# Optimization experiments

Measured on AMD Instinct MI355X. Metric: run time of the kernel, lower is better.

The kernel has to match this reference:

```python
import jax, jax.numpy as jnp
import numpy as np

B, K, C = 512, 64, 2048  # batch, mixture components, copy (eval points)


def setup_inputs() -> dict:
    key = jax.random.key(0)
    kw, km, ks, kr, kx = jax.random.split(key, 5)
    w = jax.random.uniform(kw, (B, K), dtype=jnp.float32)            # mixture weights
    means = jax.random.normal(km, (B, K, 2), dtype=jnp.float32)      # mean1, mean2
    sds = jax.random.uniform(ks, (B, K, 2), dtype=jnp.float32,
                             minval=0.5, maxval=1.5)                 # sd1, sd2 (>0)
    corr = jax.random.uniform(kr, (B, K), dtype=jnp.float32,
                              minval=-0.8, maxval=0.8)               # |corr| < 1
    model_out = jnp.concatenate(
        [w[..., None], means, sds, corr[..., None]], axis=-1)        # [B, K, 6]
    X = jax.random.normal(kx, (B, C, 2), dtype=jnp.float32)
    return {"model_out": model_out, "X": X}


def reference(model_out, X):
    # Unpack params: w, mean1, mean2, sd1, sd2, corr  -- each [B, K]
    w = model_out[..., 0]
    m1 = model_out[..., 1]
    m2 = model_out[..., 2]
    s1 = model_out[..., 3]
    s2 = model_out[..., 4]
    r = model_out[..., 5]

    # Closed-form bivariate normal pdf (equivalent to Cholesky-based
    # MultivariateNormal log_prob for the 2x2 covariance built in torch).
    # dx, dy: [B, C, K] via broadcasting X[B,C,1] against params[B,1,K]
    dx = (X[:, :, 0:1] - m1[:, None, :]) / s1[:, None, :]
    dy = (X[:, :, 1:2] - m2[:, None, :]) / s2[:, None, :]
    rb = r[:, None, :]
    omr2 = 1.0 - rb * rb  # 1 - rho^2
    z = dx * dx - 2.0 * rb * dx * dy + dy * dy
    two_pi = 2.0 * jnp.pi
    norm = two_pi * s1[:, None, :] * s2[:, None, :] * jnp.sqrt(omr2)
    probs = jnp.exp(-0.5 * z / omr2) / norm  # [B, C, K]

    # Weighted sum over components -> [B, C]
    return jnp.einsum('bck,bk->bc', probs, w)
```

## Files before the change

kernel.cpp:

```cpp
#include <hip/hip_runtime.h>
#include <hip/hip_bf16.h>


typedef float v2f __attribute__((ext_vector_type(2)));

constexpr int B = 512;
constexpr int K = 64;
constexpr int C = 2048;
constexpr int BLOCK = 256;
constexpr int HALVES = 2;
constexpr int CH = C / HALVES;

__global__ __launch_bounds__(256) void prep_kernel(
    const float* __restrict__ mo,
    float* __restrict__ P)
{
    const int i = blockIdx.x * 256 + threadIdx.x;
    const float* p = mo + (size_t)i * 6;
    const float w  = p[0];
    const float m1 = p[1];
    const float m2 = p[2];
    const float s1 = p[3];
    const float s2 = p[4];
    const float r  = p[5];

    const float omr2 = fmaf(-r, r, 1.0f);
    const float inv  = 1.0f / omr2;
    const float a2   = 0.7213475204444817f * inv;
    const float sc   = sqrtf(a2);
    const float is1  = sc / s1;
    const float is2  = sc / s2;
    const float nm1  = -(m1 * is1);
    const float nm2  = -(m2 * is2);
    const float r2   = 2.0f * r;
    const float wn   = w * 0.15915494309189535f / (s1 * s2 * sqrtf(omr2));

    float4* q = (float4*)(P + (size_t)i * 16);
    q[0] = make_float4(is1, is1, is2, is2);
    q[1] = make_float4(nm1, nm1, nm2, nm2);
    q[2] = make_float4(r2, r2, wn, wn);
}

__global__ __launch_bounds__(BLOCK) void mixture_kernel(
    const float* __restrict__ X,
    const float* __restrict__ P,
    float* __restrict__ out)
{
    const int bid = blockIdx.x;
    const int b   = bid >> 1;
    const int h   = bid & 1;
    const int t   = threadIdx.x;

    const float4* Xb = (const float4*)(X + (size_t)b * C * 2 + (size_t)h * CH * 2);
    const float4 xv0 = Xb[t];
    const float4 xv1 = Xb[t + BLOCK];

    const v2f xs0 = { xv0.x, xv0.z };
    const v2f ys0 = { xv0.y, xv0.w };
    const v2f xs1 = { xv1.x, xv1.z };
    const v2f ys1 = { xv1.y, xv1.w };
    v2f acc0 = { 0.0f, 0.0f };
    v2f acc1 = { 0.0f, 0.0f };

    const v2f* __restrict__ Pb = (const v2f*)(P + (size_t)b * K * 16);

#pragma unroll 4
    for (int k = 0; k < K; ++k) {
        const v2f IS1 = Pb[k * 8 + 0];
        const v2f IS2 = Pb[k * 8 + 1];
        const v2f NM1 = Pb[k * 8 + 2];
        const v2f NM2 = Pb[k * 8 + 3];
        const v2f R2  = Pb[k * 8 + 4];
        const v2f WN  = Pb[k * 8 + 5];

        {
            const v2f dx = __builtin_elementwise_fma(xs0, IS1, NM1);
            const v2f dy = __builtin_elementwise_fma(ys0, IS2, NM2);
            const v2f pq = dx * dy;
            v2f u        = dx * dx;
            u            = __builtin_elementwise_fma(dy, dy, u);
            const v2f e  = __builtin_elementwise_fma(R2, pq, -u);
            v2f ex;
            ex.x = __builtin_amdgcn_exp2f(e.x);
            ex.y = __builtin_amdgcn_exp2f(e.y);
            acc0 = __builtin_elementwise_fma(WN, ex, acc0);
        }
        {
            const v2f dx = __builtin_elementwise_fma(xs1, IS1, NM1);
            const v2f dy = __builtin_elementwise_fma(ys1, IS2, NM2);
            const v2f pq = dx * dy;
            v2f u        = dx * dx;
            u            = __builtin_elementwise_fma(dy, dy, u);
            const v2f e  = __builtin_elementwise_fma(R2, pq, -u);
            v2f ex;
            ex.x = __builtin_amdgcn_exp2f(e.x);
            ex.y = __builtin_amdgcn_exp2f(e.y);
            acc1 = __builtin_elementwise_fma(WN, ex, acc1);
        }
    }

    float2* ob = (float2*)(out + (size_t)b * C + (size_t)h * CH);
    ob[t]         = make_float2(acc0.x, acc0.y);
    ob[t + BLOCK] = make_float2(acc1.x, acc1.y);
}

extern "C" void kernel_launch(void* const* d_in, const int* in_sizes, int n_in,
                              void* d_out, int out_size, void* d_ws, size_t ws_size,
                              hipStream_t stream) {
    const float* mo = (const float*)d_in[0];
    const float* X  = (const float*)d_in[1];
    float* out      = (float*)d_out;
    float* P        = (float*)d_ws;

    prep_kernel<<<dim3(B * K / 256), dim3(256), 0, stream>>>(mo, P);
    mixture_kernel<<<dim3(B * HALVES), dim3(BLOCK), 0, stream>>>(X, P, out);
}
```

Baseline: 79.64 us.

## Fuse parameter prep into mixture kernel and broadcast params via readlane

Removes the separate prep kernel and its workspace round-trip: each wavefront lane computes the derived parameters for one mixture component, and the inner loop broadcasts them with readlane into scalar registers. This eliminates one kernel launch and the global-memory loads of the packed parameter table. In exchange every wave redundantly recomputes the 64 components' parameters (divisions, sqrts), and the loop unroll is raised to 8.

```diff
diff --git a/kernel.cpp b/kernel.cpp
--- a/kernel.cpp
+++ b/kernel.cpp
@@ -1,5 +1,4 @@
 #include <hip/hip_runtime.h>
-#include <hip/hip_bf16.h>
 
 
 typedef float v2f __attribute__((ext_vector_type(2)));
@@ -11,12 +10,26 @@
 constexpr int HALVES = 2;
 constexpr int CH = C / HALVES;
 
-__global__ __launch_bounds__(256) void prep_kernel(
+__device__ __forceinline__ float rdlane(float v, int k) {
+    return __uint_as_float(__builtin_amdgcn_readlane(__float_as_uint(v), k));
+}
+
+__global__ __launch_bounds__(BLOCK) void mixture_kernel(
     const float* __restrict__ mo,
-    float* __restrict__ P)
+    const float* __restrict__ X,
+    float* __restrict__ out)
 {
-    const int i = blockIdx.x * 256 + threadIdx.x;
-    const float* p = mo + (size_t)i * 6;
+    const int bid = blockIdx.x;
+    const int b   = bid >> 1;
+    const int h   = bid & 1;
+    const int t   = threadIdx.x;
+    const int lane = t & 63;
+
+    const float4* Xb = (const float4*)(X + (size_t)b * C * 2 + (size_t)h * CH * 2);
+    const float4 xv0 = Xb[t];
+    const float4 xv1 = Xb[t + BLOCK];
+
+    const float* p = mo + ((size_t)(b * K + lane)) * 6;
     const float w  = p[0];
     const float m1 = p[1];
     const float m2 = p[2];
@@ -28,32 +41,12 @@
     const float inv  = 1.0f / omr2;
     const float a2   = 0.7213475204444817f * inv;
     const float sc   = sqrtf(a2);
-    const float is1  = sc / s1;
-    const float is2  = sc / s2;
-    const float nm1  = -(m1 * is1);
-    const float nm2  = -(m2 * is2);
-    const float r2   = 2.0f * r;
-    const float wn   = w * 0.15915494309189535f / (s1 * s2 * sqrtf(omr2));
-
-    float4* q = (float4*)(P + (size_t)i * 16);
-    q[0] = make_float4(is1, is1, is2, is2);
-    q[1] = make_float4(nm1, nm1, nm2, nm2);
-    q[2] = make_float4(r2, r2, wn, wn);
-}
-
-__global__ __launch_bounds__(BLOCK) void mixture_kernel(
-    const float* __restrict__ X,
-    const float* __restrict__ P,
-    float* __restrict__ out)
-{
-    const int bid = blockIdx.x;
-    const int b   = bid >> 1;
-    const int h   = bid & 1;
-    const int t   = threadIdx.x;
-
-    const float4* Xb = (const float4*)(X + (size_t)b * C * 2 + (size_t)h * CH * 2);
-    const float4 xv0 = Xb[t];
-    const float4 xv1 = Xb[t + BLOCK];
+    const float cIS1 = sc / s1;
+    const float cIS2 = sc / s2;
+    const float cNM1 = -(m1 * cIS1);
+    const float cNM2 = -(m2 * cIS2);
+    const float cR2  = 2.0f * r;
+    const float cWN  = w * 0.15915494309189535f * sqrtf(inv) / (s1 * s2);
 
     const v2f xs0 = { xv0.x, xv0.z };
     const v2f ys0 = { xv0.y, xv0.w };
@@ -62,16 +55,21 @@
     v2f acc0 = { 0.0f, 0.0f };
     v2f acc1 = { 0.0f, 0.0f };
 
-    const v2f* __restrict__ Pb = (const v2f*)(P + (size_t)b * K * 16);
+#pragma unroll 8
+    for (int k = 0; k < K; ++k) {
+        const float fIS1 = rdlane(cIS1, k);
+        const float fIS2 = rdlane(cIS2, k);
+        const float fNM1 = rdlane(cNM1, k);
+        const float fNM2 = rdlane(cNM2, k);
+        const float fR2  = rdlane(cR2, k);
+        const float fWN  = rdlane(cWN, k);
 
-#pragma unroll 4
-    for (int k = 0; k < K; ++k) {
-        const v2f IS1 = Pb[k * 8 + 0];
-        const v2f IS2 = Pb[k * 8 + 1];
-        const v2f NM1 = Pb[k * 8 + 2];
-        const v2f NM2 = Pb[k * 8 + 3];
-        const v2f R2  = Pb[k * 8 + 4];
-        const v2f WN  = Pb[k * 8 + 5];
+        const v2f IS1 = { fIS1, fIS1 };
+        const v2f IS2 = { fIS2, fIS2 };
+        const v2f NM1 = { fNM1, fNM1 };
+        const v2f NM2 = { fNM2, fNM2 };
+        const v2f R2  = { fR2, fR2 };
+        const v2f WN  = { fWN, fWN };
 
         {
             const v2f dx = __builtin_elementwise_fma(xs0, IS1, NM1);
@@ -110,8 +108,6 @@
     const float* mo = (const float*)d_in[0];
     const float* X  = (const float*)d_in[1];
     float* out      = (float*)d_out;
-    float* P        = (float*)d_ws;
 
-    prep_kernel<<<dim3(B * K / 256), dim3(256), 0, stream>>>(mo, P);
-    mixture_kernel<<<dim3(B * HALVES), dim3(BLOCK), 0, stream>>>(X, P, out);
+    mixture_kernel<<<dim3(B * HALVES), dim3(BLOCK), 0, stream>>>(mo, X, out);
 }
```

Result: faster. 77.55 us (-2.6%).
